# Optimization experiments

Measured on AMD Instinct MI355X. Metric: run time of the kernel, lower is better.

## Reference

```python
import jax, jax.numpy as jnp
import numpy as np

H = 16          # num_heads
D = 64          # head_dim = dim // num_heads
ROPE_THETA = 10000.0
NEG = -1e9


def _rope_angles(n, d):
    # matches get_1d_rotary_pos_embed(head_dim, N): freqs_cis = polar(1, t outer (theta^-(2i/d)))
    inv_freq = 1.0 / (ROPE_THETA ** (jnp.arange(0, d, 2, dtype=jnp.float32) / d))  # [d/2]
    ang = jnp.arange(n, dtype=jnp.float32)[:, None] * inv_freq[None, :]            # [n, d/2]
    return jnp.cos(ang), jnp.sin(ang)


def _apply_rope(x, cos, sin):
    # x: [B,H,N,D]; complex rotation on adjacent pairs (use_real=False semantics)
    x0 = x[..., 0::2]
    x1 = x[..., 1::2]
    # broadcast cos/sin [N, D/2] over batch and heads
    r0 = x0 * cos - x1 * sin
    r1 = x0 * sin + x1 * cos
    return jnp.stack([r0, r1], axis=-1).reshape(x.shape)


def setup_inputs() -> dict:
    key = jax.random.key(0)
    ks = jax.random.split(key, 5)
    B, N, C = 4, 2048, 1024
    s_in = 1.0 / np.sqrt(C)
    return {
        "x": jax.random.normal(ks[0], (B, N, C), dtype=jnp.float32),
        "Wqkv_w": jax.random.normal(ks[1], (3 * C, C), dtype=jnp.float32) * s_in,
        "Wqkv_b": jax.random.normal(ks[2], (3 * C,), dtype=jnp.float32) * 0.01,
        "out_w": jax.random.normal(ks[3], (C, C), dtype=jnp.float32) * s_in,
        "out_b": jax.random.normal(ks[4], (C,), dtype=jnp.float32) * 0.01,
    }


def reference(x, Wqkv_w, Wqkv_b, out_w, out_b):
    B, N, C = x.shape
    scale = D ** -0.5
    # fused QKV projection: [B,N,3C] -> [3,B,H,N,D]
    qkv = (jnp.einsum('bnc,oc->bno', x, Wqkv_w) + Wqkv_b)
    qkv = qkv.reshape(B, N, 3, H, D).transpose(2, 0, 3, 1, 4)
    q, k, v = qkv[0], qkv[1], qkv[2]
    # qk_norm=False -> Identity
    cos, sin = _rope_angles(N, D)
    q = _apply_rope(q, cos, sin)
    k = _apply_rope(k, cos, sin)
    attn = jnp.einsum('bhqd,bhkd->bhqk', q * scale, k)      # [B,H,N,N]
    causal = jnp.triu(jnp.ones((N, N), dtype=bool), k=1)
    attn = jnp.where(causal[None, None], NEG, attn)
    attn = jax.nn.softmax(attn, axis=-1)
    o = jnp.einsum('bhqk,bhkd->bhqd', attn, v)              # [B,H,N,D]
    o = o.transpose(0, 2, 1, 3).reshape(B, N, C)
    return jnp.einsum('bnc,oc->bno', o, out_w) + out_b
```

## Files before the change

kernel.cpp:

```cpp
#include <hip/hip_runtime.h>
#include <hip/hip_bf16.h>

#define DEVI __device__ __forceinline__

typedef __attribute__((ext_vector_type(8))) short short8v;
typedef __attribute__((ext_vector_type(4))) float f32x4;
typedef __attribute__((ext_vector_type(16))) float f32x16;
typedef __attribute__((ext_vector_type(2))) unsigned u32x2;
typedef __attribute__((ext_vector_type(4))) unsigned u32x4;

DEVI short f2bf(float f) {
  __hip_bfloat16 h = __float2bfloat16(f);
  return __builtin_bit_cast(short, h);
}
DEVI float bf2f(short s) {
  unsigned u = ((unsigned)(unsigned short)s) << 16;
  return __builtin_bit_cast(float, u);
}
DEVI unsigned packbf(float a, float b) {
  return (unsigned)(unsigned short)f2bf(a) | ((unsigned)(unsigned short)f2bf(b) << 16);
}
DEVI void gload16(const void* g, void* l) {
  __builtin_amdgcn_global_load_lds((const __attribute__((address_space(1))) void*)g,
                                   (__attribute__((address_space(3))) void*)l, 16, 0, 0);
}
#define MFMA16(a, b, c) __builtin_amdgcn_mfma_f32_16x16x32_bf16((a), (b), (c), 0, 0, 0)
#define MFMA32(a, b, c) __builtin_amdgcn_mfma_f32_32x32x16_bf16((a), (b), (c), 0, 0, 0)
#define PLSWAP(a, b) asm("v_permlane32_swap_b32 %0, %1" : "+v"(a), "+v"(b))


__global__ void cvt_all(const float* __restrict__ x, const float* __restrict__ wq,
                        const float* __restrict__ wo, short* __restrict__ xb,
                        short* __restrict__ wqb, short* __restrict__ wob) {
  int i = blockIdx.x * blockDim.x + threadIdx.x;
  const float* in;
  short* out;
  if (i < 2097152) { in = x; out = xb; }
  else if (i < 2097152 + 786432) { in = wq; out = wqb; i -= 2097152; }
  else { in = wo; out = wob; i -= 2097152 + 786432; }
  float4 v = ((const float4*)in)[i];
  short4 o;
  o.x = f2bf(v.x); o.y = f2bf(v.y); o.z = f2bf(v.z); o.w = f2bf(v.w);
  ((short4*)out)[i] = o;
}

__global__ void rope_table(float2* __restrict__ tbl) {
  int i = blockIdx.x * blockDim.x + threadIdx.x;
  int n = i >> 5, f = i & 31;
  float inv = powf(10000.0f, -(float)f * (1.0f / 32.0f));
  float ang = (float)n * inv;
  tbl[i] = make_float2(cosf(ang), sinf(ang));
}

__global__ void rope_k(short* __restrict__ kk, const float2* __restrict__ tbl) {
  int i = blockIdx.x * blockDim.x + threadIdx.x;
  int row = i >> 3, c8 = i & 7;
  int n = row & 2047;
  short* ad = kk + (size_t)row * 64 + c8 * 8;
  short8v vv = *(short8v*)ad;
  short8v ov;
#pragma unroll
  for (int j = 0; j < 4; ++j) {
    float2 cs = tbl[n * 32 + c8 * 4 + j];
    float x0 = bf2f(vv[2 * j]), x1 = bf2f(vv[2 * j + 1]);
    ov[2 * j]     = f2bf(x0 * cs.x - x1 * cs.y);
    ov[2 * j + 1] = f2bf(x0 * cs.y + x1 * cs.x);
  }
  *(short8v*)ad = ov;
}

__global__ __launch_bounds__(512, 2)
void gemm256(const short* __restrict__ A, const short* __restrict__ Bw,
             const float* __restrict__ bias,
             short* __restrict__ q, short* __restrict__ k, short* __restrict__ v,
             int Kdim) {
  __shared__ __attribute__((aligned(16))) short lds[65536];
  const int t = threadIdx.x;
  const int lane = t & 63, w = t >> 6;
  const int wr = w >> 2, wc = w & 3;
  const int g = lane >> 4, r16 = lane & 15;

  const int flat = blockIdx.y * 12 + blockIdx.x;
  const int swz = (flat & 7) * 48 + (flat >> 3);
  const int n0 = (swz % 12) * 256, m0 = (swz / 12) * 256;

  int goffs[4], loffs[4];
#pragma unroll
  for (int p = 0; p < 4; ++p) {
    int c = p * 512 + t;
    int row = c >> 3, u = c & 7;
    goffs[p] = row * Kdim + ((u ^ (row & 7)) * 8);
    loffs[p] = c * 16;
  }
  const short* Abase = A + (size_t)m0 * Kdim;
  const short* Bbase = Bw + (size_t)n0 * Kdim;

  auto STAGE = [&](int s, int k0) {
#pragma unroll
    for (int p = 0; p < 4; ++p) {
      gload16(Abase + k0 + goffs[p], (char*)lds + s * 32768 + loffs[p]);
      gload16(Bbase + k0 + goffs[p], (char*)lds + 65536 + s * 32768 + loffs[p]);
    }
  };

  f32x4 acc[8][4];
#pragma unroll
  for (int i = 0; i < 8; ++i)
#pragma unroll
    for (int j = 0; j < 4; ++j) acc[i][j] = (f32x4){0.f, 0.f, 0.f, 0.f};

  const int nsteps = Kdim >> 6;
  STAGE(0, 0);
  __syncthreads();

  int cur = 0;
  for (int st = 0; st < nsteps; ++st) {
    if (st + 1 < nsteps) STAGE(cur ^ 1, (st + 1) << 6);
    const char* Ab = (const char*)lds + cur * 32768;
    const char* Bb = (const char*)lds + 65536 + cur * 32768;
#pragma unroll
    for (int ks = 0; ks < 2; ++ks) {
      short8v bf[4];
#pragma unroll
      for (int ni = 0; ni < 4; ++ni) {
        int rowb = wc * 64 + ni * 16 + r16;
        bf[ni] = *(const short8v*)(Bb + rowb * 128 + (((ks * 4 + g) ^ (rowb & 7)) << 4));
      }
#pragma unroll
      for (int mi = 0; mi < 8; ++mi) {
        int rowa = wr * 128 + mi * 16 + r16;
        short8v af =
            *(const short8v*)(Ab + rowa * 128 + (((ks * 4 + g) ^ (rowa & 7)) << 4));
#pragma unroll
        for (int ni = 0; ni < 4; ++ni)
          acc[mi][ni] = MFMA16(af, bf[ni], acc[mi][ni]);
      }
    }
    __syncthreads();
    cur ^= 1;
  }

  const int b = m0 >> 11, nb = m0 & 2047;
  if (n0 < 2048) {
#pragma unroll
    for (int ni = 0; ni < 4; ++ni) {
      int col = n0 + wc * 64 + ni * 16 + r16;
      float bv = bias[col];
      int s = col >> 10, h = (col & 1023) >> 6, d = col & 63;
      short* dst = (s == 0) ? q : k;
#pragma unroll
      for (int mi = 0; mi < 8; ++mi) {
        int mrow = m0 + wr * 128 + mi * 16 + g * 4;
#pragma unroll
        for (int r = 0; r < 4; ++r) {
          int n = (mrow + r) & 2047;
          dst[(((size_t)(b * 16 + h)) * 2048 + n) * 64 + d] = f2bf(acc[mi][ni][r] + bv);
        }
      }
    }
  } else {
    short* Cs = lds;
    const int hdrb = (n0 - 2048) >> 6;
#pragma unroll
    for (int hh = 0; hh < 4; ++hh) {
      if (wc == hh) {
#pragma unroll
        for (int ni = 0; ni < 4; ++ni) {
          float bv = bias[n0 + hh * 64 + ni * 16 + r16];
#pragma unroll
          for (int mi = 0; mi < 8; ++mi) {
            u32x2 pk;
            pk[0] = packbf(acc[mi][ni][0] + bv, acc[mi][ni][1] + bv);
            pk[1] = packbf(acc[mi][ni][2] + bv, acc[mi][ni][3] + bv);
            *(u32x2*)&Cs[(ni * 16 + r16) * 264 + wr * 128 + mi * 16 + g * 4] = pk;
          }
        }
      }
      __syncthreads();
      short* vdst = v + ((size_t)(b * 16 + hdrb + hh)) * 64 * 2048;
#pragma unroll
      for (int j = 0; j < 4; ++j) {
        int chunk = j * 512 + t;
        int d = chunk >> 5, c = chunk & 31;
        short8v val = *(const short8v*)&Cs[d * 264 + c * 8];
        *(short8v*)(vdst + (size_t)d * 2048 + nb + c * 8) = val;
      }
      __syncthreads();
    }
  }
}

__global__ __launch_bounds__(256)
void gemm_f32(const short* __restrict__ A, const short* __restrict__ Bw,
              const float* __restrict__ bias, float* __restrict__ fout,
              int Ndim, int Kdim) {
  __shared__ __attribute__((aligned(16))) short As[3][128 * 32];
  __shared__ __attribute__((aligned(16))) short Bs[3][128 * 32];
  const int t = threadIdx.x;
  const int lane = t & 63, w = t >> 6;
  const int wr = w >> 1, wc = w & 1;
  const int g = lane >> 4, r16 = lane & 15;
  const int m0 = blockIdx.y * 128, n0 = blockIdx.x * 128;

  int goffs[2], loffs[2];
#pragma unroll
  for (int p = 0; p < 2; ++p) {
    int c = p * 256 + t;
    int row = c >> 2, u = c & 3;
    goffs[p] = row * Kdim + ((u ^ ((row >> 1) & 3)) * 8);
    loffs[p] = c * 16;
  }
  const short* Abase = A + (size_t)m0 * Kdim;
  const short* Bbase = Bw + (size_t)n0 * Kdim;

  auto STAGE = [&](int s, int k0) {
#pragma unroll
    for (int p = 0; p < 2; ++p) {
      gload16(Abase + k0 + goffs[p], (char*)&As[s][0] + loffs[p]);
      gload16(Bbase + k0 + goffs[p], (char*)&Bs[s][0] + loffs[p]);
    }
  };

  f32x4 acc[4][4];
#pragma unroll
  for (int i = 0; i < 4; ++i)
#pragma unroll
    for (int j = 0; j < 4; ++j) acc[i][j] = (f32x4){0.f, 0.f, 0.f, 0.f};

  const int nsteps = Kdim >> 5;
  STAGE(0, 0);
  STAGE(1, 32);
  asm volatile("s_waitcnt vmcnt(4)" ::: "memory");
  __builtin_amdgcn_s_barrier();
  asm volatile("" ::: "memory");

  int cur = 0, pre = 2;
  const int rsw = (r16 >> 1) & 3;
  for (int st = 0; st < nsteps; ++st) {
    if (st + 2 < nsteps) STAGE(pre, (st + 2) << 5);
    short8v af[4], bf[4];
#pragma unroll
    for (int mi = 0; mi < 4; ++mi)
      af[mi] = *(const short8v*)&As[cur][(wr * 64 + mi * 16 + r16) * 32 +
                                         ((g ^ rsw) * 8)];
#pragma unroll
    for (int ni = 0; ni < 4; ++ni)
      bf[ni] = *(const short8v*)&Bs[cur][(wc * 64 + ni * 16 + r16) * 32 +
                                         ((g ^ rsw) * 8)];
#pragma unroll
    for (int mi = 0; mi < 4; ++mi)
#pragma unroll
      for (int ni = 0; ni < 4; ++ni)
        acc[mi][ni] = MFMA16(af[mi], bf[ni], acc[mi][ni]);
    if (st + 2 < nsteps) asm volatile("s_waitcnt vmcnt(4)" ::: "memory");
    else                 asm volatile("s_waitcnt vmcnt(0)" ::: "memory");
    __builtin_amdgcn_s_barrier();
    asm volatile("" ::: "memory");
    cur = (cur == 2) ? 0 : cur + 1;
    pre = (pre == 2) ? 0 : pre + 1;
  }

#pragma unroll
  for (int ni = 0; ni < 4; ++ni) {
    int col = n0 + wc * 64 + ni * 16 + r16;
    float bv = bias[col];
#pragma unroll
    for (int mi = 0; mi < 4; ++mi) {
      int mrow = m0 + wr * 64 + mi * 16 + g * 4;
#pragma unroll
      for (int r = 0; r < 4; ++r)
        fout[(size_t)(mrow + r) * Ndim + col] = acc[mi][ni][r] + bv;
    }
  }
}

__global__ __launch_bounds__(512)
void fattn(const short* __restrict__ q, const short* __restrict__ k,
           const short* __restrict__ vT, const float2* __restrict__ tbl,
           short* __restrict__ o) {
  const int bx = blockIdx.x;
  const int idx = bx >> 6;
  const int qt = (idx < 4) ? (7 - idx) : (idx - 4);
  const int bh = bx & 63;
  const int b = bh >> 4, h = bh & 15;
  const int t = threadIdx.x, lane = t & 63, w = t >> 6;
  const int q32 = lane & 31, hi = lane >> 5;
  const int hi4 = hi * 4;

  __shared__ __attribute__((aligned(16))) short Ks[2][64 * 64];
  __shared__ __attribute__((aligned(16))) short Vt[2][64 * 64];

  const short* qb = q + (size_t)bh * 2048 * 64;
  const short* kb = k + (size_t)bh * 2048 * 64;
  const short* vb = vT + (size_t)bh * 2048 * 64;

  const int srow = t >> 3, su = t & 7;
  const int sx8 = (su ^ (srow & 7)) * 8;
  const int koff = srow * 64 + sx8;
  const int voff = srow * 2048 + sx8;
  const int loff = t * 16;
  auto STAGE = [&](int s, int kt) {
    gload16(kb + (size_t)kt * 4096 + koff, (char*)&Ks[s][0] + loff);
    gload16(vb + kt * 64 + voff, (char*)&Vt[s][0] + loff);
  };

  const int q0w = qt * 256 + w * 32;
  const int nrow = q0w + q32;

  const float sc = 0.125f * 1.44269504088896f;
  short8v aq[4];
#pragma unroll
  for (int ds = 0; ds < 4; ++ds) {
    short8v raw = *(const short8v*)(qb + (size_t)nrow * 64 + ds * 16 + hi * 8);
    short8v rq;
#pragma unroll
    for (int j = 0; j < 4; ++j) {
      float2 cs = tbl[nrow * 32 + ds * 8 + hi4 + j];
      float x0 = bf2f(raw[2 * j]), x1 = bf2f(raw[2 * j + 1]);
      rq[2 * j]     = f2bf((x0 * cs.x - x1 * cs.y) * sc);
      rq[2 * j + 1] = f2bf((x0 * cs.y + x1 * cs.x) * sc);
    }
    aq[ds] = rq;
  }

  const short one_bf = 0x3F80;
  const short8v ones = {one_bf, one_bf, one_bf, one_bf, one_bf, one_bf, one_bf, one_bf};
  const float M = 24.0f;

  f32x16 oacc[2], lacc;
#pragma unroll
  for (int j = 0; j < 16; ++j) { oacc[0][j] = 0.f; oacc[1][j] = 0.f; lacc[j] = 0.f; }

  const int ktmax = 4 * qt + 3;

  STAGE(0, 0);
  __syncthreads();

  for (int kt = 0; kt <= ktmax; ++kt) {
    const int cur = kt & 1;
    if (kt < ktmax) STAGE(cur ^ 1, kt + 1);

    if (kt * 64 <= q0w + 31) {
      f32x16 s[2];
#pragma unroll
      for (int j = 0; j < 16; ++j) { s[0][j] = 0.f; s[1][j] = 0.f; }
      __builtin_amdgcn_s_setprio(1);
#pragma unroll
      for (int ds = 0; ds < 4; ++ds) {
        int u = 2 * ds + hi;
#pragma unroll
        for (int kbl = 0; kbl < 2; ++kbl) {
          int key = kbl * 32 + q32;
          short8v kf = *(const short8v*)((const char*)&Ks[cur][0] + key * 128 +
                                         ((u ^ (key & 7)) << 4));
          s[kbl] = MFMA32(kf, aq[ds], s[kbl]);
        }
      }
      __builtin_amdgcn_s_setprio(0);

      const bool needmask = (kt * 64 + 63 > q0w);
      unsigned pa[4][4];
#pragma unroll
      for (int kbl = 0; kbl < 2; ++kbl) {
        if (needmask) {
#pragma unroll
          for (int r = 0; r < 16; ++r) {
            int keyg = kt * 64 + kbl * 32 + (r & 3) + 8 * (r >> 2) + hi4;
            if (keyg > nrow) s[kbl][r] = -1e30f;
          }
        }
        unsigned pk[8];
#pragma unroll
        for (int p = 0; p < 8; ++p) {
          float p0 = __builtin_amdgcn_exp2f(s[kbl][2 * p] - M);
          float p1 = __builtin_amdgcn_exp2f(s[kbl][2 * p + 1] - M);
          pk[p] = packbf(p0, p1);
        }
        {
          unsigned x0 = pk[0], x1 = pk[2];
          unsigned y0 = pk[1], y1 = pk[3];
          PLSWAP(x0, x1);
          PLSWAP(y0, y1);
          pa[kbl * 2][0] = x0; pa[kbl * 2][1] = y0;
          pa[kbl * 2][2] = x1; pa[kbl * 2][3] = y1;
        }
        {
          unsigned x0 = pk[4], x1 = pk[6];
          unsigned y0 = pk[5], y1 = pk[7];
          PLSWAP(x0, x1);
          PLSWAP(y0, y1);
          pa[kbl * 2 + 1][0] = x0; pa[kbl * 2 + 1][1] = y0;
          pa[kbl * 2 + 1][2] = x1; pa[kbl * 2 + 1][3] = y1;
        }
      }

      __builtin_amdgcn_s_setprio(1);
#pragma unroll
      for (int kk = 0; kk < 4; ++kk) {
        short8v paf = __builtin_bit_cast(
            short8v, (u32x4){pa[kk][0], pa[kk][1], pa[kk][2], pa[kk][3]});
        lacc = MFMA32(paf, ones, lacc);
        int u = 2 * kk + hi;
#pragma unroll
        for (int db = 0; db < 2; ++db) {
          int d = db * 32 + q32;
          short8v vf = *(const short8v*)((const char*)&Vt[cur][0] + d * 128 +
                                         ((u ^ (d & 7)) << 4));
          oacc[db] = MFMA32(paf, vf, oacc[db]);
        }
      }
      __builtin_amdgcn_s_setprio(0);
    }
    __syncthreads();
  }

#pragma unroll
  for (int r = 0; r < 16; ++r) {
    float ilr = 1.f / lacc[r];
    int qg = q0w + (r & 3) + 8 * (r >> 2) + hi4;
    short* orow = o + ((size_t)(b * 2048 + qg)) * 1024 + h * 64;
    orow[q32]      = f2bf(oacc[0][r] * ilr);
    orow[32 + q32] = f2bf(oacc[1][r] * ilr);
  }
}

extern "C" void kernel_launch(void* const* d_in, const int* in_sizes, int n_in,
                              void* d_out, int out_size, void* d_ws, size_t ws_size,
                              hipStream_t stream) {
  const float* x    = (const float*)d_in[0];
  const float* Wqkv = (const float*)d_in[1];
  const float* bqkv = (const float*)d_in[2];
  const float* Wout = (const float*)d_in[3];
  const float* bout = (const float*)d_in[4];

  char* p = (char*)d_ws;
  short* xb = (short*)p;    p += (size_t)8192 * 1024 * 2;
  short* wqkvb = (short*)p; p += (size_t)3072 * 1024 * 2;
  short* woutb = (short*)p; p += (size_t)1024 * 1024 * 2;
  short* qbf = (short*)p;   p += (size_t)64 * 2048 * 64 * 2;
  short* kbf = (short*)p;   p += (size_t)64 * 2048 * 64 * 2;
  short* vbf = (short*)p;   p += (size_t)64 * 2048 * 64 * 2;
  float2* tbl = (float2*)p; p += (size_t)2048 * 32 * 8;

  cvt_all<<<12288, 256, 0, stream>>>(x, Wqkv, Wout, xb, wqkvb, woutb);
  rope_table<<<256, 256, 0, stream>>>(tbl);

  gemm256<<<dim3(12, 32), 512, 0, stream>>>(xb, wqkvb, bqkv, qbf, kbf, vbf, 1024);
  rope_k<<<4096, 256, 0, stream>>>(kbf, tbl);
  fattn<<<dim3(512), 512, 0, stream>>>(qbf, kbf, vbf, tbl, xb);
  gemm_f32<<<dim3(8, 64), 256, 0, stream>>>(xb, woutb, bout, (float*)d_out, 1024, 1024);
}
```

Before: 182.5 us.

## Enlarge out-projection GEMM tile and skip fully masked key blocks in attention

The output-projection GEMM now uses 256x128 tiles with each wave computing 128x64, on a two-stage LDS double buffer instead of three stages. The launch grid is halved to match. In attention, the second 32-key sub-block is skipped when it lies entirely above the causal diagonal. The max offset is folded into the score accumulator's initial value, and P·V is fused per key sub-block. The intent is more operand reuse per LDS load and less wasted masked work, at the cost of fewer GEMM blocks (256) and shallower prefetch.

```diff
diff --git a/kernel.cpp b/kernel.cpp
--- a/kernel.cpp
+++ b/kernel.cpp
@@ -194,70 +194,73 @@
 void gemm_f32(const short* __restrict__ A, const short* __restrict__ Bw,
               const float* __restrict__ bias, float* __restrict__ fout,
               int Ndim, int Kdim) {
-  __shared__ __attribute__((aligned(16))) short As[3][128 * 32];
-  __shared__ __attribute__((aligned(16))) short Bs[3][128 * 32];
+  __shared__ __attribute__((aligned(16))) short As[2][256 * 32];
+  __shared__ __attribute__((aligned(16))) short Bs[2][128 * 32];
   const int t = threadIdx.x;
   const int lane = t & 63, w = t >> 6;
   const int wr = w >> 1, wc = w & 1;
   const int g = lane >> 4, r16 = lane & 15;
-  const int m0 = blockIdx.y * 128, n0 = blockIdx.x * 128;
-
-  int goffs[2], loffs[2];
+  const int m0 = blockIdx.y * 256, n0 = blockIdx.x * 128;
+
+  int goffA[4], loffA[4], goffB[2], loffB[2];
+#pragma unroll
+  for (int p = 0; p < 4; ++p) {
+    int c = p * 256 + t;
+    int row = c >> 2, u = c & 3;
+    goffA[p] = row * Kdim + ((u ^ ((row >> 1) & 3)) * 8);
+    loffA[p] = c * 16;
+  }
 #pragma unroll
   for (int p = 0; p < 2; ++p) {
     int c = p * 256 + t;
     int row = c >> 2, u = c & 3;
-    goffs[p] = row * Kdim + ((u ^ ((row >> 1) & 3)) * 8);
-    loffs[p] = c * 16;
+    goffB[p] = row * Kdim + ((u ^ ((row >> 1) & 3)) * 8);
+    loffB[p] = c * 16;
   }
   const short* Abase = A + (size_t)m0 * Kdim;
   const short* Bbase = Bw + (size_t)n0 * Kdim;
 
   auto STAGE = [&](int s, int k0) {
 #pragma unroll
-    for (int p = 0; p < 2; ++p) {
-      gload16(Abase + k0 + goffs[p], (char*)&As[s][0] + loffs[p]);
-      gload16(Bbase + k0 + goffs[p], (char*)&Bs[s][0] + loffs[p]);
-    }
+    for (int p = 0; p < 4; ++p)
+      gload16(Abase + k0 + goffA[p], (char*)&As[s][0] + loffA[p]);
+#pragma unroll
+    for (int p = 0; p < 2; ++p)
+      gload16(Bbase + k0 + goffB[p], (char*)&Bs[s][0] + loffB[p]);
   };
 
-  f32x4 acc[4][4];
-#pragma unroll
-  for (int i = 0; i < 4; ++i)
+  f32x4 acc[8][4];
+#pragma unroll
+  for (int i = 0; i < 8; ++i)
 #pragma unroll
     for (int j = 0; j < 4; ++j) acc[i][j] = (f32x4){0.f, 0.f, 0.f, 0.f};
 
   const int nsteps = Kdim >> 5;
   STAGE(0, 0);
-  STAGE(1, 32);
-  asm volatile("s_waitcnt vmcnt(4)" ::: "memory");
-  __builtin_amdgcn_s_barrier();
-  asm volatile("" ::: "memory");
-
-  int cur = 0, pre = 2;
+  __syncthreads();
+
   const int rsw = (r16 >> 1) & 3;
+  int cur = 0;
   for (int st = 0; st < nsteps; ++st) {
-    if (st + 2 < nsteps) STAGE(pre, (st + 2) << 5);
-    short8v af[4], bf[4];
-#pragma unroll
-    for (int mi = 0; mi < 4; ++mi)
-      af[mi] = *(const short8v*)&As[cur][(wr * 64 + mi * 16 + r16) * 32 +
-                                         ((g ^ rsw) * 8)];
-#pragma unroll
-    for (int ni = 0; ni < 4; ++ni)
-      bf[ni] = *(const short8v*)&Bs[cur][(wc * 64 + ni * 16 + r16) * 32 +
-                                         ((g ^ rsw) * 8)];
-#pragma unroll
-    for (int mi = 0; mi < 4; ++mi)
+    if (st + 1 < nsteps) STAGE(cur ^ 1, (st + 1) << 5);
+    short8v bf[4];
+#pragma unroll
+    for (int ni = 0; ni < 4; ++ni) {
+      int rowb = wc * 64 + ni * 16 + r16;
+      bf[ni] = *(const short8v*)((const char*)&Bs[cur][0] + rowb * 64 +
+                                 ((g ^ rsw) << 4));
+    }
+#pragma unroll
+    for (int mi = 0; mi < 8; ++mi) {
+      int rowa = wr * 128 + mi * 16 + r16;
+      short8v af = *(const short8v*)((const char*)&As[cur][0] + rowa * 64 +
+                                     ((g ^ rsw) << 4));
 #pragma unroll
       for (int ni = 0; ni < 4; ++ni)
-        acc[mi][ni] = MFMA16(af[mi], bf[ni], acc[mi][ni]);
-    if (st + 2 < nsteps) asm volatile("s_waitcnt vmcnt(4)" ::: "memory");
-    else                 asm volatile("s_waitcnt vmcnt(0)" ::: "memory");
-    __builtin_amdgcn_s_barrier();
-    asm volatile("" ::: "memory");
-    cur = (cur == 2) ? 0 : cur + 1;
-    pre = (pre == 2) ? 0 : pre + 1;
+        acc[mi][ni] = MFMA16(af, bf[ni], acc[mi][ni]);
+    }
+    __syncthreads();
+    cur ^= 1;
   }
 
 #pragma unroll
@@ -265,8 +268,8 @@
     int col = n0 + wc * 64 + ni * 16 + r16;
     float bv = bias[col];
 #pragma unroll
-    for (int mi = 0; mi < 4; ++mi) {
-      int mrow = m0 + wr * 64 + mi * 16 + g * 4;
+    for (int mi = 0; mi < 8; ++mi) {
+      int mrow = m0 + wr * 128 + mi * 16 + g * 4;
 #pragma unroll
       for (int r = 0; r < 4; ++r)
         fout[(size_t)(mrow + r) * Ndim + col] = acc[mi][ni][r] + bv;
@@ -341,15 +344,18 @@
     if (kt < ktmax) STAGE(cur ^ 1, kt + 1);
 
     if (kt * 64 <= q0w + 31) {
+      const bool skip1 = (kt * 64 + 32 > q0w + 31);
+
       f32x16 s[2];
 #pragma unroll
-      for (int j = 0; j < 16; ++j) { s[0][j] = 0.f; s[1][j] = 0.f; }
+      for (int j = 0; j < 16; ++j) { s[0][j] = -M; s[1][j] = -M; }
       __builtin_amdgcn_s_setprio(1);
 #pragma unroll
       for (int ds = 0; ds < 4; ++ds) {
         int u = 2 * ds + hi;
 #pragma unroll
         for (int kbl = 0; kbl < 2; ++kbl) {
+          if (kbl == 1 && skip1) continue;
           int key = kbl * 32 + q32;
           short8v kf = *(const short8v*)((const char*)&Ks[cur][0] + key * 128 +
                                          ((u ^ (key & 7)) << 4));
@@ -359,9 +365,9 @@
       __builtin_amdgcn_s_setprio(0);
 
       const bool needmask = (kt * 64 + 63 > q0w);
-      unsigned pa[4][4];
 #pragma unroll
       for (int kbl = 0; kbl < 2; ++kbl) {
+        if (kbl == 1 && skip1) continue;
         if (needmask) {
 #pragma unroll
           for (int r = 0; r < 16; ++r) {
@@ -372,44 +378,35 @@
         unsigned pk[8];
 #pragma unroll
         for (int p = 0; p < 8; ++p) {
-          float p0 = __builtin_amdgcn_exp2f(s[kbl][2 * p] - M);
-          float p1 = __builtin_amdgcn_exp2f(s[kbl][2 * p + 1] - M);
+          float p0 = __builtin_amdgcn_exp2f(s[kbl][2 * p]);
+          float p1 = __builtin_amdgcn_exp2f(s[kbl][2 * p + 1]);
           pk[p] = packbf(p0, p1);
         }
-        {
-          unsigned x0 = pk[0], x1 = pk[2];
-          unsigned y0 = pk[1], y1 = pk[3];
-          PLSWAP(x0, x1);
-          PLSWAP(y0, y1);
-          pa[kbl * 2][0] = x0; pa[kbl * 2][1] = y0;
-          pa[kbl * 2][2] = x1; pa[kbl * 2][3] = y1;
-        }
-        {
-          unsigned x0 = pk[4], x1 = pk[6];
-          unsigned y0 = pk[5], y1 = pk[7];
-          PLSWAP(x0, x1);
-          PLSWAP(y0, y1);
-          pa[kbl * 2 + 1][0] = x0; pa[kbl * 2 + 1][1] = y0;
-          pa[kbl * 2 + 1][2] = x1; pa[kbl * 2 + 1][3] = y1;
-        }
-      }
-
-      __builtin_amdgcn_s_setprio(1);
-#pragma unroll
-      for (int kk = 0; kk < 4; ++kk) {
-        short8v paf = __builtin_bit_cast(
-            short8v, (u32x4){pa[kk][0], pa[kk][1], pa[kk][2], pa[kk][3]});
-        lacc = MFMA32(paf, ones, lacc);
-        int u = 2 * kk + hi;
+        unsigned x0 = pk[0], x1 = pk[2], y0 = pk[1], y1 = pk[3];
+        PLSWAP(x0, x1);
+        PLSWAP(y0, y1);
+        unsigned z0 = pk[4], z1 = pk[6], w0 = pk[5], w1 = pk[7];
+        PLSWAP(z0, z1);
+        PLSWAP(w0, w1);
+        short8v paf0 = __builtin_bit_cast(short8v, (u32x4){x0, y0, x1, y1});
+        short8v paf1 = __builtin_bit_cast(short8v, (u32x4){z0, w0, z1, w1});
+
+        __builtin_amdgcn_s_setprio(1);
+        lacc = MFMA32(paf0, ones, lacc);
+        lacc = MFMA32(paf1, ones, lacc);
+        const int u0 = 2 * (2 * kbl) + hi, u1 = 2 * (2 * kbl + 1) + hi;
 #pragma unroll
         for (int db = 0; db < 2; ++db) {
           int d = db * 32 + q32;
-          short8v vf = *(const short8v*)((const char*)&Vt[cur][0] + d * 128 +
-                                         ((u ^ (d & 7)) << 4));
-          oacc[db] = MFMA32(paf, vf, oacc[db]);
-        }
-      }
-      __builtin_amdgcn_s_setprio(0);
+          short8v vf0 = *(const short8v*)((const char*)&Vt[cur][0] + d * 128 +
+                                          ((u0 ^ (d & 7)) << 4));
+          oacc[db] = MFMA32(paf0, vf0, oacc[db]);
+          short8v vf1 = *(const short8v*)((const char*)&Vt[cur][0] + d * 128 +
+                                          ((u1 ^ (d & 7)) << 4));
+          oacc[db] = MFMA32(paf1, vf1, oacc[db]);
+        }
+        __builtin_amdgcn_s_setprio(0);
+      }
     }
     __syncthreads();
   }
@@ -448,5 +445,5 @@
   gemm256<<<dim3(12, 32), 512, 0, stream>>>(xb, wqkvb, bqkv, qbf, kbf, vbf, 1024);
   rope_k<<<4096, 256, 0, stream>>>(kbf, tbl);
   fattn<<<dim3(512), 512, 0, stream>>>(qbf, kbf, vbf, tbl, xb);
-  gemm_f32<<<dim3(8, 64), 256, 0, stream>>>(xb, woutb, bout, (float*)d_out, 1024, 1024);
-}
+  gemm_f32<<<dim3(8, 32), 256, 0, stream>>>(xb, woutb, bout, (float*)d_out, 1024, 1024);
+}
```

Measured after the change: 198.4 us. 8.7% more time.
